# Kernel optimization log

Measured on AMD Instinct MI355X. Metric: run time of the kernel, lower is better.

## Reference

```python
import jax, jax.numpy as jnp
import numpy as np

N_NODES = 50000
N_EDGES = 800000
IN_DIM = 100
HID = 128
OUT = 128
EPS = 1e-5


def setup_inputs() -> dict:
    key = jax.random.key(0)
    ks = jax.random.split(key, 12)
    x = jax.random.normal(ks[0], (N_NODES, IN_DIM), dtype=jnp.float32)
    edge_index = jax.random.randint(ks[1], (2, N_EDGES), 0, N_NODES, dtype=jnp.int32)
    def lin(k, i, o):
        return jax.random.normal(k, (i, o), dtype=jnp.float32) * (1.0 / np.sqrt(i))
    return {
        "x": x,
        "edge_index": edge_index,
        "W_l0": lin(ks[2], IN_DIM, HID),  # neighbor transform, layer 0
        "b_l0": jnp.zeros((HID,), jnp.float32),
        "W_r0": lin(ks[3], IN_DIM, HID),  # root transform, layer 0
        "gamma0": jnp.ones((HID,), jnp.float32),
        "beta0": jnp.zeros((HID,), jnp.float32),
        "W_l1": lin(ks[4], HID, OUT),
        "b_l1": jnp.zeros((OUT,), jnp.float32),
        "W_r1": lin(ks[5], HID, OUT),
        "gamma1": jnp.ones((OUT,), jnp.float32),
        "beta1": jnp.zeros((OUT,), jnp.float32),
    }


def _sage_conv(x, edge_index, W_l, b_l, W_r):
    # PyG SAGEConv (mean aggr): out = lin_l(mean_{j->i} x_j) + lin_r(x_i)
    src, dst = edge_index[0], edge_index[1]
    n = x.shape[0]
    msg_sum = jax.ops.segment_sum(x[src], dst, num_segments=n)        # [N, d_in]
    cnt = jax.ops.segment_sum(jnp.ones((src.shape[0],), x.dtype), dst, num_segments=n)
    agg = msg_sum / jnp.maximum(cnt, 1.0)[:, None]
    return agg @ W_l + b_l + x @ W_r


def _batch_norm(x, gamma, beta):
    # BatchNorm1d with batch statistics (training-mode math, biased var)
    mean = x.mean(axis=0)
    var = x.var(axis=0)
    return gamma * (x - mean) / jnp.sqrt(var + EPS) + beta


def reference(x, edge_index, W_l0, b_l0, W_r0, gamma0, beta0, W_l1, b_l1, W_r1, gamma1, beta1):
    # Layer 0: SAGEConv -> BN -> ReLU (dropout off for determinism)
    h = _sage_conv(x, edge_index, W_l0, b_l0, W_r0)
    h = jax.nn.relu(_batch_norm(h, gamma0, beta0))
    # Layer 1 (last): SAGEConv -> BN
    h = _sage_conv(h, edge_index, W_l1, b_l1, W_r1)
    return _batch_norm(h, gamma1, beta1)
```

## Files before the change

### kernel.cpp

```cpp
#include <hip/hip_runtime.h>
#include <hip/hip_bf16.h>

#define N_NODES 50000
#define N_EDGES 800000
#define BSHIFT  5
#define BUCKS   1563
#define NPAD    50016
#define BSTRIDE 1024
#define BCAP    1024
#define IN_DIM  100
#define HID     128
#define BN_EPS  1e-5f
#define NSLICE  32

#define SC_BLKS 98
#define CAST_ELEMS (NPAD * 128 + 4 * 16384)
#define CAST_BLKS ((CAST_ELEMS + 4095) / 4096)

typedef unsigned int uint;
typedef unsigned short u16;
typedef __attribute__((ext_vector_type(8))) unsigned short us8;
typedef __attribute__((ext_vector_type(8))) short s8;
typedef __attribute__((ext_vector_type(16))) float f16v;
typedef __attribute__((ext_vector_type(4))) float f4;

__device__ __forceinline__ u16 f2bf(float f) {
    uint u = __builtin_bit_cast(uint, f);
    uint r = (u + 0x7FFFu + ((u >> 16) & 1u)) >> 16;
    return (u16)r;
}
__device__ __forceinline__ uint pack2(float a, float b) {
    return (uint)f2bf(a) | ((uint)f2bf(b) << 16);
}
__device__ __forceinline__ float bflo(uint p) { return __builtin_bit_cast(float, p << 16); }
__device__ __forceinline__ float bfhi(uint p) { return __builtin_bit_cast(float, p & 0xFFFF0000u); }
__device__ __forceinline__ float bfu(u16 v) { return __builtin_bit_cast(float, (uint)v << 16); }

template <typename T>
__device__ __forceinline__ T ntload(const T* p) {
    return __builtin_nontemporal_load(const_cast<T*>(p));
}
template <typename T>
__device__ __forceinline__ void ntstore(T* p, T v) {
    __builtin_nontemporal_store(v, p);
}

__global__ __launch_bounds__(1024) void scatter_cast(
    const int* __restrict__ src, const int* __restrict__ dst,
    int* __restrict__ bcursor, uint* __restrict__ ebuf,
    const float* __restrict__ x,
    const float* __restrict__ W_l0, const float* __restrict__ W_r0,
    const float* __restrict__ W_l1, const float* __restrict__ W_r1,
    u16* __restrict__ xb, u16* __restrict__ Wt) {
    __shared__ int h[BUCKS];
    __shared__ int gb[BUCKS];
    int t = threadIdx.x;

    if (blockIdx.x >= SC_BLKS) {
        int base = (blockIdx.x - SC_BLKS) * 4096 + t;
        #pragma unroll
        for (int r = 0; r < 4; ++r) {
            int idx = base + r * 1024;
            if (idx < NPAD * 128) {
                int row = idx >> 7, k = idx & 127;
                float v = (row < N_NODES && k < IN_DIM) ? ntload(x + row * IN_DIM + k) : 0.f;
                ntstore(xb + idx, f2bf(v));
            } else if (idx < CAST_ELEMS) {
                int i2 = idx - NPAD * 128;
                int w = i2 >> 14, i3 = i2 & 16383;
                const float* s = (w == 0) ? W_l0 : (w == 1) ? W_r0 : (w == 2) ? W_l1 : W_r1;
                int Ks = (w < 2) ? IN_DIM : HID;
                int n = i3 >> 7, k = i3 & 127;
                float v = (k < Ks) ? s[k * 128 + n] : 0.f;
                Wt[i2] = f2bf(v);
            }
        }
        return;
    }

    for (int i = t; i < BUCKS; i += 1024) h[i] = 0;
    __syncthreads();
    int base = blockIdx.x * 8192;
    int myb[8]; uint myv[8];
    #pragma unroll
    for (int r = 0; r < 8; ++r) {
        int e = base + r * 1024 + t;
        int b = -1; uint val = 0;
        if (e < N_EDGES) {
            int d = ntload(dst + e);
            b = d >> BSHIFT;
            val = (uint)ntload(src + e) | ((uint)(d & 31) << 16);
            atomicAdd(&h[b], 1);
        }
        myb[r] = b; myv[r] = val;
    }
    __syncthreads();
    for (int i = t; i < BUCKS; i += 1024) {
        int c = h[i];
        gb[i] = c ? (i * BSTRIDE + atomicAdd(&bcursor[i], c)) : 0;
        h[i] = 0;
    }
    __syncthreads();
    #pragma unroll
    for (int r = 0; r < 8; ++r) {
        int b = myb[r];
        if (b >= 0) {
            int pos = gb[b] + atomicAdd(&h[b], 1);
            ntstore(ebuf + pos, myv[r]);
        }
    }
}

template <int APPLY_BN, int WRITE_BF16>
__global__ __launch_bounds__(256) void agg_gemm(
    const uint* __restrict__ ebuf, const int* __restrict__ bcursor,
    const u16* __restrict__ X,
    const u16* __restrict__ WtL, const u16* __restrict__ WtR,
    const float* __restrict__ bias,
    float* __restrict__ outf, u16* __restrict__ outb,
    float* __restrict__ gstats_out,
    const float* __restrict__ gstats_in,
    const float* __restrict__ gamma, const float* __restrict__ beta,
    float inv_n) {
    __shared__ u16 Aagg[32][136];
    __shared__ uint eL[BCAP];
    __shared__ u16 srcL[BCAP];
    __shared__ int cnt[32], ro[33], cur[32];
    __shared__ float s1L[128], s2L[128];
    __shared__ float ss[256];

    int b = blockIdx.x;
    int t = threadIdx.x;
    int row0 = b * 32;
    int wave = t >> 6, lane = t & 63;
    int quad = lane >> 4, sub = lane & 15;

    if (APPLY_BN && t < 128) {
        float m = 0.f, q = 0.f;
        #pragma unroll
        for (int s = 0; s < NSLICE; ++s) {
            m += gstats_in[s * 256 + t];
            q += gstats_in[s * 256 + 128 + t];
        }
        float mean = m * inv_n;
        float var = q * inv_n - mean * mean;
        float inv = 1.0f / sqrtf(var + BN_EPS);
        float sc = gamma[t] * inv;
        ss[t] = sc;
        ss[128 + t] = beta[t] - mean * sc;
    }

    int n = bcursor[b];
    if (n > BCAP) n = BCAP;
    if (t < 32) cnt[t] = 0;
    if (t < 128) { s1L[t] = 0.f; s2L[t] = 0.f; }
    __syncthreads();
    for (int i = t; i < n; i += 256) {
        uint p = ntload(ebuf + b * BSTRIDE + i);
        eL[i] = p;
        atomicAdd(&cnt[p >> 16], 1);
    }
    __syncthreads();
    if (t < 32) {
        int v = cnt[t];
        int s = v;
        #pragma unroll
        for (int off = 1; off < 32; off <<= 1) {
            int u = __shfl_up(s, off, 64);
            if (t >= off) s += u;
        }
        ro[t] = s - v;
        cur[t] = s - v;
        if (t == 31) ro[32] = s;
    }
    __syncthreads();
    for (int i = t; i < n; i += 256) {
        uint p = eL[i];
        int pos = atomicAdd(&cur[p >> 16], 1);
        srcL[pos] = (u16)(p & 0xFFFFu);
    }
    __syncthreads();

    float scr[8], shr[8];
    if (APPLY_BN) {
        #pragma unroll
        for (int j = 0; j < 8; ++j) {
            scr[j] = ss[sub * 8 + j];
            shr[j] = ss[128 + sub * 8 + j];
        }
    }
    int nl0 = (wave * 4 + quad) * 2;
    #pragma unroll
    for (int g = 0; g < 2; ++g) {
        int nl = nl0 + g;
        int rb = ro[nl], re = ro[nl + 1];
        float a[8];
        #pragma unroll
        for (int j = 0; j < 8; ++j) a[j] = 0.f;

        auto acc1 = [&](uint4 v) {
            float f[8] = { bflo(v.x), bfhi(v.x), bflo(v.y), bfhi(v.y),
                           bflo(v.z), bfhi(v.z), bflo(v.w), bfhi(v.w) };
            #pragma unroll
            for (int j = 0; j < 8; ++j) {
                float val = f[j];
                if (APPLY_BN) val = fmaxf(fmaf(val, scr[j], shr[j]), 0.f);
                a[j] += val;
            }
        };

        int e = rb;
        for (; e + 4 <= re; e += 4) {
            int s0 = srcL[e], s1 = srcL[e + 1], s2 = srcL[e + 2], s3 = srcL[e + 3];
            uint4 v0 = ((const uint4*)(X + (size_t)s0 * 128))[sub];
            uint4 v1 = ((const uint4*)(X + (size_t)s1 * 128))[sub];
            uint4 v2 = ((const uint4*)(X + (size_t)s2 * 128))[sub];
            uint4 v3 = ((const uint4*)(X + (size_t)s3 * 128))[sub];
            acc1(v0); acc1(v1); acc1(v2); acc1(v3);
        }
        for (; e < re; ++e) {
            uint4 v0 = ((const uint4*)(X + (size_t)srcL[e] * 128))[sub];
            acc1(v0);
        }
        float inv = 1.0f / fmaxf((float)(re - rb), 1.0f);
        uint4 o;
        o.x = pack2(a[0] * inv, a[1] * inv);
        o.y = pack2(a[2] * inv, a[3] * inv);
        o.z = pack2(a[4] * inv, a[5] * inv);
        o.w = pack2(a[6] * inv, a[7] * inv);
        *(uint4*)&Aagg[nl][sub * 8] = o;
    }
    __syncthreads();

    int m31 = lane & 31;
    int kh  = lane >> 5;
    int cn = wave * 32;
    f16v acc = (f16v)0.f;

    {
        s8 a_nxt = *(const s8*)&Aagg[m31][kh * 8];
        s8 b_nxt = *(const s8*)(WtL + (cn + m31) * 128 + kh * 8);
        #pragma unroll
        for (int ks = 0; ks < 8; ++ks) {
            s8 a_cur = a_nxt, b_cur = b_nxt;
            if (ks < 7) {
                a_nxt = *(const s8*)&Aagg[m31][(ks + 1) * 16 + kh * 8];
                b_nxt = *(const s8*)(WtL + (cn + m31) * 128 + (ks + 1) * 16 + kh * 8);
            }
            acc = __builtin_amdgcn_mfma_f32_32x32x16_bf16(a_cur, b_cur, acc, 0, 0, 0);
        }
    }
    {
        const u16* xrow = X + (size_t)(row0 + m31) * 128;
        us8 a_nxt = *(const us8*)(xrow + kh * 8);
        s8 b_nxt = *(const s8*)(WtR + (cn + m31) * 128 + kh * 8);
        #pragma unroll
        for (int ks = 0; ks < 8; ++ks) {
            us8 a_raw = a_nxt;
            s8 b_cur = b_nxt;
            if (ks < 7) {
                a_nxt = *(const us8*)(xrow + (ks + 1) * 16 + kh * 8);
                b_nxt = *(const s8*)(WtR + (cn + m31) * 128 + (ks + 1) * 16 + kh * 8);
            }
            s8 a_cur;
            if (APPLY_BN) {
                int kb = ks * 16 + kh * 8;
                #pragma unroll
                for (int j = 0; j < 8; ++j) {
                    float f = bfu(a_raw[j]);
                    f = fmaxf(fmaf(f, ss[kb + j], ss[128 + kb + j]), 0.f);
                    a_cur[j] = (short)f2bf(f);
                }
            } else {
                a_cur = __builtin_bit_cast(s8, a_raw);
            }
            acc = __builtin_amdgcn_mfma_f32_32x32x16_bf16(a_cur, b_cur, acc, 0, 0, 0);
        }
    }

    {
        int col = cn + m31;
        float bv = bias[col];
        float s1 = 0.f, s2 = 0.f;
        #pragma unroll
        for (int reg = 0; reg < 16; ++reg) {
            int rowin = (reg & 3) + 8 * (reg >> 2) + 4 * kh;
            int row = row0 + rowin;
            if (row < N_NODES) {
                float v = acc[reg] + bv;
                if (WRITE_BF16)
                    ntstore(outb + (size_t)row * 128 + col, f2bf(v));
                else
                    ntstore(outf + (size_t)row * 128 + col, v);
                s1 += v;
                s2 = fmaf(v, v, s2);
            }
        }
        s1 += __shfl_xor(s1, 32, 64);
        s2 += __shfl_xor(s2, 32, 64);
        if (lane < 32) {
            atomicAdd(&s1L[col], s1);
            atomicAdd(&s2L[col], s2);
        }
    }
    __syncthreads();
    int slice = b & (NSLICE - 1);
    if (t < 128) {
        atomicAdd(&gstats_out[slice * 256 + t], s1L[t]);
        atomicAdd(&gstats_out[slice * 256 + 128 + t], s2L[t]);
    }
}

__global__ void bn_apply_kernel(float* __restrict__ h,
                                const float* __restrict__ gstats,
                                const float* __restrict__ gamma,
                                const float* __restrict__ beta,
                                float inv_n, int total4) {
    __shared__ float ss[256];
    int t = threadIdx.x;
    if (t < 128) {
        float m = 0.f, q = 0.f;
        #pragma unroll
        for (int s = 0; s < NSLICE; ++s) {
            m += gstats[s * 256 + t];
            q += gstats[s * 256 + 128 + t];
        }
        float mean = m * inv_n;
        float var = q * inv_n - mean * mean;
        float inv = 1.0f / sqrtf(var + BN_EPS);
        float sc = gamma[t] * inv;
        ss[t] = sc;
        ss[128 + t] = beta[t] - mean * sc;
    }
    __syncthreads();
    for (int i = blockIdx.x * 256 + t; i < total4; i += gridDim.x * 256) {
        int cg = i & 31;
        f4 v = ((const f4*)h)[i];
        f4 sc = *(const f4*)&ss[cg * 4];
        f4 sh = *(const f4*)&ss[128 + cg * 4];
        v.x = fmaf(v.x, sc.x, sh.x);
        v.y = fmaf(v.y, sc.y, sh.y);
        v.z = fmaf(v.z, sc.z, sh.z);
        v.w = fmaf(v.w, sc.w, sh.w);
        ntstore(((f4*)h) + i, v);
    }
}

extern "C" void kernel_launch(void* const* d_in, const int* in_sizes, int n_in,
                              void* d_out, int out_size, void* d_ws, size_t ws_size,
                              hipStream_t stream) {
    const float* x      = (const float*)d_in[0];
    const int*   ei     = (const int*)d_in[1];
    const float* W_l0   = (const float*)d_in[2];
    const float* b_l0   = (const float*)d_in[3];
    const float* W_r0   = (const float*)d_in[4];
    const float* gamma0 = (const float*)d_in[5];
    const float* beta0  = (const float*)d_in[6];
    const float* W_l1   = (const float*)d_in[7];
    const float* b_l1   = (const float*)d_in[8];
    const float* W_r1   = (const float*)d_in[9];
    const float* gamma1 = (const float*)d_in[10];
    const float* beta1  = (const float*)d_in[11];

    const int* src = ei;
    const int* dst = ei + N_EDGES;

    char* w = (char*)d_ws;
    auto alloc = [&](size_t bytes) {
        void* p = (void*)w;
        w += (bytes + 255) & ~(size_t)255;
        return p;
    };
    char* zbase    = w;
    float* gstats0 = (float*)alloc(sizeof(float) * NSLICE * 256);
    float* gstats1 = (float*)alloc(sizeof(float) * NSLICE * 256);
    int* bcursor   = (int*)alloc(sizeof(int) * BUCKS);
    size_t zbytes  = (size_t)(w - zbase);

    uint* ebuf     = (uint*)alloc(sizeof(uint) * (size_t)BUCKS * BSTRIDE);
    u16* xb        = (u16*)alloc(sizeof(u16) * (size_t)NPAD * 128);
    u16* hb        = (u16*)alloc(sizeof(u16) * (size_t)NPAD * 128);
    u16* Wt        = (u16*)alloc(sizeof(u16) * 4 * 16384);
    float* outp    = (float*)d_out;

    hipMemsetAsync(zbase, 0, zbytes, stream);

    const float inv_n = 1.0f / (float)N_NODES;
    const int total4 = N_NODES * HID / 4;

    scatter_cast<<<SC_BLKS + CAST_BLKS, 1024, 0, stream>>>(
        src, dst, bcursor, ebuf, x, W_l0, W_r0, W_l1, W_r1, xb, Wt);

    agg_gemm<0, 1><<<BUCKS, 256, 0, stream>>>(
        ebuf, bcursor, xb, Wt, Wt + 16384, b_l0,
        nullptr, hb, gstats0, nullptr, nullptr, nullptr, inv_n);

    agg_gemm<1, 0><<<BUCKS, 256, 0, stream>>>(
        ebuf, bcursor, hb, Wt + 2 * 16384, Wt + 3 * 16384, b_l1,
        outp, nullptr, gstats1, gstats0, gamma0, beta0, inv_n);

    bn_apply_kernel<<<2048, 256, 0, stream>>>(outp, gstats1, gamma1, beta1, inv_n, total4);
}
```

Measured before the change: 237.2 us.

## Halve rows per aggregation block to 16 and use 32-bit gather offsets

Buckets shrink from 32 to 16 destination rows, doubling the number of agg_gemm blocks to 3125, and each quad now aggregates one row instead of two. The upper 16 rows of the MFMA A tile are zeroed, and the row bounds check on output is removed because 3125*16 equals N_NODES exactly. Gather addresses are computed as 32-bit byte offsets, and non-temporal loads and stores are dropped in a few places. The aim is more parallelism and less per-thread serial gather work. In exchange, half of each MFMA tile is wasted on zero rows and per-block overhead is duplicated across twice as many blocks.

```diff
diff --git a/kernel.cpp b/kernel.cpp
--- a/kernel.cpp
+++ b/kernel.cpp
@@ -3,18 +3,19 @@
 
 #define N_NODES 50000
 #define N_EDGES 800000
-#define BSHIFT  5
-#define BUCKS   1563
-#define NPAD    50016
-#define BSTRIDE 1024
-#define BCAP    1024
+#define BSHIFT  4
+#define NROW    16
+#define BUCKS   3125
+#define NPALLOC 50016
+#define BSTRIDE 512
+#define BCAP    512
 #define IN_DIM  100
 #define HID     128
 #define BN_EPS  1e-5f
 #define NSLICE  32
 
 #define SC_BLKS 98
-#define CAST_ELEMS (NPAD * 128 + 4 * 16384)
+#define CAST_ELEMS (NPALLOC * 128 + 4 * 16384)
 #define CAST_BLKS ((CAST_ELEMS + 4095) / 4096)
 
 typedef unsigned int uint;
@@ -22,7 +23,6 @@
 typedef __attribute__((ext_vector_type(8))) unsigned short us8;
 typedef __attribute__((ext_vector_type(8))) short s8;
 typedef __attribute__((ext_vector_type(16))) float f16v;
-typedef __attribute__((ext_vector_type(4))) float f4;
 
 __device__ __forceinline__ u16 f2bf(float f) {
     uint u = __builtin_bit_cast(uint, f);
@@ -61,12 +61,12 @@
         #pragma unroll
         for (int r = 0; r < 4; ++r) {
             int idx = base + r * 1024;
-            if (idx < NPAD * 128) {
+            if (idx < NPALLOC * 128) {
                 int row = idx >> 7, k = idx & 127;
-                float v = (row < N_NODES && k < IN_DIM) ? ntload(x + row * IN_DIM + k) : 0.f;
+                float v = (row < N_NODES && k < IN_DIM) ? x[row * IN_DIM + k] : 0.f;
                 ntstore(xb + idx, f2bf(v));
             } else if (idx < CAST_ELEMS) {
-                int i2 = idx - NPAD * 128;
+                int i2 = idx - NPALLOC * 128;
                 int w = i2 >> 14, i3 = i2 & 16383;
                 const float* s = (w == 0) ? W_l0 : (w == 1) ? W_r0 : (w == 2) ? W_l1 : W_r1;
                 int Ks = (w < 2) ? IN_DIM : HID;
@@ -87,9 +87,9 @@
         int e = base + r * 1024 + t;
         int b = -1; uint val = 0;
         if (e < N_EDGES) {
-            int d = ntload(dst + e);
+            int d = dst[e];
             b = d >> BSHIFT;
-            val = (uint)ntload(src + e) | ((uint)(d & 31) << 16);
+            val = (uint)src[e] | ((uint)(d & (NROW - 1)) << 16);
             atomicAdd(&h[b], 1);
         }
         myb[r] = b; myv[r] = val;
@@ -125,15 +125,21 @@
     __shared__ u16 Aagg[32][136];
     __shared__ uint eL[BCAP];
     __shared__ u16 srcL[BCAP];
-    __shared__ int cnt[32], ro[33], cur[32];
+    __shared__ int cnt[NROW], ro[NROW + 1], cur[NROW];
     __shared__ float s1L[128], s2L[128];
     __shared__ float ss[256];
 
     int b = blockIdx.x;
     int t = threadIdx.x;
-    int row0 = b * 32;
+    int row0 = b * NROW;
     int wave = t >> 6, lane = t & 63;
     int quad = lane >> 4, sub = lane & 15;
+
+    {
+        int zr = 16 + (t >> 4), zc = (t & 15) * 8;
+        uint4 z; z.x = 0; z.y = 0; z.z = 0; z.w = 0;
+        *(uint4*)&Aagg[zr][zc] = z;
+    }
 
     if (APPLY_BN && t < 128) {
         float m = 0.f, q = 0.f;
@@ -152,7 +158,7 @@
 
     int n = bcursor[b];
     if (n > BCAP) n = BCAP;
-    if (t < 32) cnt[t] = 0;
+    if (t < NROW) cnt[t] = 0;
     if (t < 128) { s1L[t] = 0.f; s2L[t] = 0.f; }
     __syncthreads();
     for (int i = t; i < n; i += 256) {
@@ -161,17 +167,17 @@
         atomicAdd(&cnt[p >> 16], 1);
     }
     __syncthreads();
-    if (t < 32) {
+    if (t < NROW) {
         int v = cnt[t];
         int s = v;
         #pragma unroll
-        for (int off = 1; off < 32; off <<= 1) {
+        for (int off = 1; off < NROW; off <<= 1) {
             int u = __shfl_up(s, off, 64);
             if (t >= off) s += u;
         }
         ro[t] = s - v;
         cur[t] = s - v;
-        if (t == 31) ro[32] = s;
+        if (t == NROW - 1) ro[NROW] = s;
     }
     __syncthreads();
     for (int i = t; i < n; i += 256) {
@@ -189,10 +195,8 @@
             shr[j] = ss[128 + sub * 8 + j];
         }
     }
-    int nl0 = (wave * 4 + quad) * 2;
-    #pragma unroll
-    for (int g = 0; g < 2; ++g) {
-        int nl = nl0 + g;
+    {
+        int nl = wave * 4 + quad;
         int rb = ro[nl], re = ro[nl + 1];
         float a[8];
         #pragma unroll
@@ -209,17 +213,22 @@
             }
         };
 
+        const char* Xc = (const char*)X;
+        uint boff = (uint)sub * 16u;
         int e = rb;
         for (; e + 4 <= re; e += 4) {
-            int s0 = srcL[e], s1 = srcL[e + 1], s2 = srcL[e + 2], s3 = srcL[e + 3];
-            uint4 v0 = ((const uint4*)(X + (size_t)s0 * 128))[sub];
-            uint4 v1 = ((const uint4*)(X + (size_t)s1 * 128))[sub];
-            uint4 v2 = ((const uint4*)(X + (size_t)s2 * 128))[sub];
-            uint4 v3 = ((const uint4*)(X + (size_t)s3 * 128))[sub];
+            uint o0 = ((uint)srcL[e]     << 8) + boff;
+            uint o1 = ((uint)srcL[e + 1] << 8) + boff;
+            uint o2 = ((uint)srcL[e + 2] << 8) + boff;
+            uint o3 = ((uint)srcL[e + 3] << 8) + boff;
+            uint4 v0 = *(const uint4*)(Xc + o0);
+            uint4 v1 = *(const uint4*)(Xc + o1);
+            uint4 v2 = *(const uint4*)(Xc + o2);
+            uint4 v3 = *(const uint4*)(Xc + o3);
             acc1(v0); acc1(v1); acc1(v2); acc1(v3);
         }
         for (; e < re; ++e) {
-            uint4 v0 = ((const uint4*)(X + (size_t)srcL[e] * 128))[sub];
+            uint4 v0 = *(const uint4*)(Xc + ((uint)srcL[e] << 8) + boff);
             acc1(v0);
         }
         float inv = 1.0f / fmaxf((float)(re - rb), 1.0f);
@@ -251,7 +260,7 @@
         }
     }
     {
-        const u16* xrow = X + (size_t)(row0 + m31) * 128;
+        const u16* xrow = X + (size_t)((uint)(row0 + m31) * 128u);
         us8 a_nxt = *(const us8*)(xrow + kh * 8);
         s8 b_nxt = *(const s8*)(WtR + (cn + m31) * 128 + kh * 8);
         #pragma unroll
@@ -283,18 +292,16 @@
         float bv = bias[col];
         float s1 = 0.f, s2 = 0.f;
         #pragma unroll
-        for (int reg = 0; reg < 16; ++reg) {
+        for (int reg = 0; reg < 8; ++reg) {
             int rowin = (reg & 3) + 8 * (reg >> 2) + 4 * kh;
             int row = row0 + rowin;
-            if (row < N_NODES) {
-                float v = acc[reg] + bv;
-                if (WRITE_BF16)
-                    ntstore(outb + (size_t)row * 128 + col, f2bf(v));
-                else
-                    ntstore(outf + (size_t)row * 128 + col, v);
-                s1 += v;
-                s2 = fmaf(v, v, s2);
-            }
+            float v = acc[reg] + bv;
+            if (WRITE_BF16)
+                ntstore(outb + (size_t)row * 128 + col, f2bf(v));
+            else
+                ntstore(outf + (size_t)row * 128 + col, v);
+            s1 += v;
+            s2 = fmaf(v, v, s2);
         }
         s1 += __shfl_xor(s1, 32, 64);
         s2 += __shfl_xor(s2, 32, 64);
@@ -335,14 +342,14 @@
     __syncthreads();
     for (int i = blockIdx.x * 256 + t; i < total4; i += gridDim.x * 256) {
         int cg = i & 31;
-        f4 v = ((const f4*)h)[i];
-        f4 sc = *(const f4*)&ss[cg * 4];
-        f4 sh = *(const f4*)&ss[128 + cg * 4];
+        float4 v = ((float4*)h)[i];
+        float4 sc = *(const float4*)&ss[cg * 4];
+        float4 sh = *(const float4*)&ss[128 + cg * 4];
         v.x = fmaf(v.x, sc.x, sh.x);
         v.y = fmaf(v.y, sc.y, sh.y);
         v.z = fmaf(v.z, sc.z, sh.z);
         v.w = fmaf(v.w, sc.w, sh.w);
-        ntstore(((f4*)h) + i, v);
+        ((float4*)h)[i] = v;
     }
 }
 
@@ -378,8 +385,8 @@
     size_t zbytes  = (size_t)(w - zbase);
 
     uint* ebuf     = (uint*)alloc(sizeof(uint) * (size_t)BUCKS * BSTRIDE);
-    u16* xb        = (u16*)alloc(sizeof(u16) * (size_t)NPAD * 128);
-    u16* hb        = (u16*)alloc(sizeof(u16) * (size_t)NPAD * 128);
+    u16* xb        = (u16*)alloc(sizeof(u16) * (size_t)NPALLOC * 128);
+    u16* hb        = (u16*)alloc(sizeof(u16) * (size_t)NPALLOC * 128);
     u16* Wt        = (u16*)alloc(sizeof(u16) * 4 * 16384);
     float* outp    = (float*)d_out;
 
```

Measured after the change: 262.9 us. 10.8% more time.
